# Optimization experiments

Measured on AMD Instinct MI355X. Metric: run time of the kernel, lower is better.

Reference implementation:

```python
import jax, jax.numpy as jnp
import numpy as np

KERNEL_SIZE = 3
STRIDE = 2

def setup_inputs() -> dict:
    key = jax.random.key(0)
    # Batch of flattened (C,H,W) images; the original flattens to a vector and
    # multiplies by a sparse Toeplitz avg-pool matrix. Equivalent dense-layout input:
    x = jax.random.normal(key, (8, 64, 512, 512), dtype=jnp.float32)
    return {"x": x}

def reference(x):
    # Faithful math of What.dot(x): strided 2D average pooling (VALID windows),
    # applied independently per channel, sum over k x k window divided by k^2.
    k, s = KERNEL_SIZE, STRIDE
    summed = jax.lax.reduce_window(
        x, 0.0, jax.lax.add,
        window_dimensions=(1, 1, k, k),
        window_strides=(1, 1, s, s),
        padding="VALID",
    )
    return summed / jnp.asarray(k * k, dtype=x.dtype)
```

## Files before the change

kernel.cpp:

```cpp
#include <hip/hip_runtime.h>


#define IN_H 512
#define IN_W 512
#define OUT_H 255
#define OUT_W 255
#define PLANES 512
#define BAND 16

__device__ __forceinline__ float4 hrow(const float* __restrict__ rp) {
    const float4 v0 = *(const float4*)(rp);
    const float4 v1 = *(const float4*)(rp + 256);
    const float  n0 = rp[4];
    const float  n1 = rp[260];
    float4 h;
    h.x = v0.x + v0.y + v0.z;
    h.y = v0.z + v0.w + n0;
    h.z = v1.x + v1.y + v1.z;
    h.w = v1.z + v1.w + n1;
    return h;
}

__global__ __launch_bounds__(256) void KeyedAvgpool2d_kernel(
    const float* __restrict__ in, float* __restrict__ out) {
    const int lane = threadIdx.x & 63;
    const int wv   = threadIdx.x >> 6;
    const int band = blockIdx.x * 4 + wv;
    const int nc   = blockIdx.y;

    const int j0 = band * BAND;
    const int j1 = min(j0 + BAND, OUT_H);

    const float* __restrict__ rp =
        in + (size_t)nc * (IN_H * IN_W) + (size_t)(2 * j0) * IN_W + 4 * lane;
    float* __restrict__ op =
        out + (size_t)nc * (OUT_H * OUT_W) + (size_t)j0 * OUT_W + 2 * lane;

    const float inv9 = 1.0f / 9.0f;

    float4 A = hrow(rp);
    for (int m = j0; m < j1; ++m) {
        rp += IN_W;
        const float4 h1 = hrow(rp);
        rp += IN_W;
        const float4 h2 = hrow(rp);
        op[0]   = (A.x + h1.x + h2.x) * inv9;
        op[1]   = (A.y + h1.y + h2.y) * inv9;
        op[128] = (A.z + h1.z + h2.z) * inv9;
        if (lane < 63)
            op[129] = (A.w + h1.w + h2.w) * inv9;
        op += OUT_W;
        A = h2;
    }
}

extern "C" void kernel_launch(void* const* d_in, const int* in_sizes, int n_in,
                              void* d_out, int out_size, void* d_ws, size_t ws_size,
                              hipStream_t stream) {
    const float* x = (const float*)d_in[0];
    float* o = (float*)d_out;

    dim3 block(256, 1, 1);
    dim3 grid(4, PLANES, 1);
    KeyedAvgpool2d_kernel<<<grid, block, 0, stream>>>(x, o);
}
```

Measured before the change: 716.8 us.

## Use lane shuffles for neighbor columns, process row pairs, nontemporal stores

Replaces the scalar neighbor-column loads with wavefront shuffles of the next lane's first element. The loop now handles two output rows per iteration, issuing eight vector loads before computing, with an unroll hint. Outputs are written with nontemporal stores to avoid polluting the cache. This aims to raise memory-level parallelism and cut redundant loads, at the cost of shuffle instructions and more register pressure.

```diff
diff --git a/kernel.cpp b/kernel.cpp
--- a/kernel.cpp
+++ b/kernel.cpp
@@ -8,11 +8,14 @@
 #define PLANES 512
 #define BAND 16
 
-__device__ __forceinline__ float4 hrow(const float* __restrict__ rp) {
-    const float4 v0 = *(const float4*)(rp);
-    const float4 v1 = *(const float4*)(rp + 256);
-    const float  n0 = rp[4];
-    const float  n1 = rp[260];
+__device__ __forceinline__ float4 ld4(const float* __restrict__ p) {
+    return *(const float4*)p;
+}
+
+__device__ __forceinline__ float4 hsum(float4 v0, float4 v1, int nxt, bool is63) {
+    float n0 = __shfl(v0.x, nxt);
+    float n1 = __shfl(v1.x, nxt);
+    if (is63) n0 = n1;
     float4 h;
     h.x = v0.x + v0.y + v0.z;
     h.y = v0.z + v0.w + n0;
@@ -21,36 +24,75 @@
     return h;
 }
 
+__device__ __forceinline__ void st_row(float* __restrict__ op, float sx, float sy,
+                                       float sz, float sw, bool not63) {
+    const float inv9 = 1.0f / 9.0f;
+    __builtin_nontemporal_store(sx * inv9, op);
+    __builtin_nontemporal_store(sy * inv9, op + 1);
+    __builtin_nontemporal_store(sz * inv9, op + 128);
+    if (not63)
+        __builtin_nontemporal_store(sw * inv9, op + 129);
+}
+
 __global__ __launch_bounds__(256) void KeyedAvgpool2d_kernel(
     const float* __restrict__ in, float* __restrict__ out) {
     const int lane = threadIdx.x & 63;
     const int wv   = threadIdx.x >> 6;
     const int band = blockIdx.x * 4 + wv;
     const int nc   = blockIdx.y;
+    const int nxt  = (lane + 1) & 63;
+    const bool is63 = (lane == 63);
 
     const int j0 = band * BAND;
     const int j1 = min(j0 + BAND, OUT_H);
+    const int nrows = j1 - j0;
 
     const float* __restrict__ rp =
         in + (size_t)nc * (IN_H * IN_W) + (size_t)(2 * j0) * IN_W + 4 * lane;
     float* __restrict__ op =
         out + (size_t)nc * (OUT_H * OUT_W) + (size_t)j0 * OUT_W + 2 * lane;
 
-    const float inv9 = 1.0f / 9.0f;
+    float4 A;
+    {
+        float4 v0 = ld4(rp), v1 = ld4(rp + 256);
+        A = hsum(v0, v1, nxt, is63);
+    }
 
-    float4 A = hrow(rp);
-    for (int m = j0; m < j1; ++m) {
-        rp += IN_W;
-        const float4 h1 = hrow(rp);
-        rp += IN_W;
-        const float4 h2 = hrow(rp);
-        op[0]   = (A.x + h1.x + h2.x) * inv9;
-        op[1]   = (A.y + h1.y + h2.y) * inv9;
-        op[128] = (A.z + h1.z + h2.z) * inv9;
-        if (lane < 63)
-            op[129] = (A.w + h1.w + h2.w) * inv9;
-        op += OUT_W;
-        A = h2;
+    const int npair = nrows >> 1;
+#pragma unroll 2
+    for (int it = 0; it < npair; ++it) {
+        const float* r1 = rp + IN_W;
+        const float* r2 = rp + 2 * IN_W;
+        const float* r3 = rp + 3 * IN_W;
+        const float* r4 = rp + 4 * IN_W;
+        float4 a1 = ld4(r1), b1 = ld4(r1 + 256);
+        float4 a2 = ld4(r2), b2 = ld4(r2 + 256);
+        float4 a3 = ld4(r3), b3 = ld4(r3 + 256);
+        float4 a4 = ld4(r4), b4 = ld4(r4 + 256);
+        rp += 4 * IN_W;
+
+        float4 h1 = hsum(a1, b1, nxt, is63);
+        float4 h2 = hsum(a2, b2, nxt, is63);
+        float4 h3 = hsum(a3, b3, nxt, is63);
+        float4 h4 = hsum(a4, b4, nxt, is63);
+
+        st_row(op, A.x + h1.x + h2.x, A.y + h1.y + h2.y,
+                   A.z + h1.z + h2.z, A.w + h1.w + h2.w, !is63);
+        st_row(op + OUT_W, h2.x + h3.x + h4.x, h2.y + h3.y + h4.y,
+                           h2.z + h3.z + h4.z, h2.w + h3.w + h4.w, !is63);
+        op += 2 * OUT_W;
+        A = h4;
+    }
+
+    if (nrows & 1) {
+        const float* r1 = rp + IN_W;
+        const float* r2 = rp + 2 * IN_W;
+        float4 a1 = ld4(r1), b1 = ld4(r1 + 256);
+        float4 a2 = ld4(r2), b2 = ld4(r2 + 256);
+        float4 h1 = hsum(a1, b1, nxt, is63);
+        float4 h2 = hsum(a2, b2, nxt, is63);
+        st_row(op, A.x + h1.x + h2.x, A.y + h1.y + h2.y,
+                   A.z + h1.z + h2.z, A.w + h1.w + h2.w, !is63);
     }
 }
 
```

Measured after the change: 748.7 us. +4.5%, slower.
